# Kernel tuning notes

Hardware: AMD Instinct MI355X
Metric: run time of the kernel (lower is better)

Reference implementation:

```python
import jax, jax.numpy as jnp
import numpy as np

B, H, L, N, F = 32, 256, 2048, 64, 32  # batch, d_model, seq len, d_state//2 complex modes, num_features


def setup_inputs() -> dict:
    key = jax.random.key(0)
    ks = jax.random.split(key, 16)
    inp = {
        "x": jax.random.normal(ks[0], (B, H, L), jnp.float32),
        "t": jax.random.normal(ks[1], (B, H), jnp.float32),
        "features": jax.random.normal(ks[2], (B, F, L), jnp.float32),
        # time_linear
        "Wt": jax.random.normal(ks[3], (H, H), jnp.float32) / np.sqrt(H),
        "bt": jnp.zeros((H,), jnp.float32),
        # LayerNorm over d_model
        "ln_g": jnp.ones((H,), jnp.float32),
        "ln_b": jnp.zeros((H,), jnp.float32),
        # S4 (diagonal / S4D parameterization, d_state=128 -> N=64 complex, bidirectional)
        "log_dt": jnp.log(jnp.full((H,), 0.01, jnp.float32))
                  + jax.random.uniform(ks[4], (H,), jnp.float32, -1.0, 1.0),
        "logA_real": jnp.log(0.5 * jnp.ones((H, N), jnp.float32)),
        "A_imag": jnp.broadcast_to(np.pi * jnp.arange(N, dtype=jnp.float32), (H, N)).copy(),
        "C_re": jax.random.normal(ks[5], (2, H, N), jnp.float32) / np.sqrt(2 * N),
        "C_im": jax.random.normal(ks[6], (2, H, N), jnp.float32) / np.sqrt(2 * N),
        "D": jax.random.normal(ks[7], (H,), jnp.float32),
        # S4 output position-wise linear
        "Wout": jax.random.normal(ks[8], (H, H), jnp.float32) / np.sqrt(H),
        "bout": jnp.zeros((H,), jnp.float32),
        # out_linear1 / out_linear2 (1x1 convs)
        "W1": jax.random.normal(ks[9], (H, H), jnp.float32) / np.sqrt(H),
        "b1": jnp.zeros((H,), jnp.float32),
        "W2": jax.random.normal(ks[10], (H, H), jnp.float32) / np.sqrt(H),
        "b2": jnp.zeros((H,), jnp.float32),
        # feature_encoder 1x1 conv
        "Wf": jax.random.normal(ks[11], (H, F), jnp.float32) / np.sqrt(F),
        "bf": jnp.zeros((H,), jnp.float32),
    }
    return inp


def _s4_block(x, t, features, Wt, bt, ln_g, ln_b, log_dt, logA_real, A_imag,
              C_re, C_im, D, Wout, bout, W1, b1, W2, b2, Wf, bf):
    Bb, Hh, Ll = x.shape
    # time conditioning: Linear(t) broadcast over length  -> (B,H,L)
    tb = t @ Wt.T + bt
    xin = x + tb[:, :, None]
    # LayerNorm over channel (d_model) axis (norm applied on transposed tensor)
    mu = jnp.mean(xin, axis=1, keepdims=True)
    var = jnp.var(xin, axis=1, keepdims=True)
    z = (xin - mu) / jnp.sqrt(var + 1e-5) * ln_g[None, :, None] + ln_b[None, :, None]
    # --- bidirectional S4 (diagonal SSM) kernel ---
    dt = jnp.exp(log_dt)                       # (H,)
    A = -jnp.exp(logA_real) + 1j * A_imag      # (H,N)
    dtA = dt[:, None] * A                      # (H,N)
    Cd = (C_re + 1j * C_im) * (jnp.exp(dtA) - 1.0) / A      # (2,H,N) discretized C
    vand = jnp.exp(dtA[:, :, None] * jnp.arange(Ll))         # (H,N,L) Vandermonde
    K = 2.0 * jnp.real(jnp.einsum('chn,hnl->chl', Cd, vand))  # (2,H,L)
    zeros = jnp.zeros_like(K[0])
    k = jnp.concatenate([K[0], zeros], -1) + jnp.concatenate([zeros, K[1][:, ::-1]], -1)  # (H,2L)
    # FFT global convolution
    y = jnp.fft.irfft(jnp.fft.rfft(z, 2 * Ll) * jnp.fft.rfft(k, 2 * Ll)[None], 2 * Ll)[..., :Ll]
    y = y + z * D[None, :, None]
    y = jax.nn.gelu(y)
    y = jnp.einsum('bhl,gh->bgl', y, Wout) + bout[None, :, None]
    xr = y + xin                                # residual inside S4Layer
    # feature encoder + gated activation
    out = xr + jnp.einsum('bfl,hf->bhl', features, Wf) + bf[None, :, None]
    g = jnp.tanh(out) * jax.nn.sigmoid(out)
    o1 = jnp.einsum('bhl,gh->bgl', g, W1) + b1[None, :, None]
    o2 = jnp.einsum('bhl,gh->bgl', g, W2) + b2[None, :, None]
    return (o1 + x, o2)


def reference(x, t, features, Wt, bt, ln_g, ln_b, log_dt, logA_real, A_imag,
              C_re, C_im, D, Wout, bout, W1, b1, W2, b2, Wf, bf):
    return _s4_block(x, t, features, Wt, bt, ln_g, ln_b, log_dt, logA_real, A_imag,
                     C_re, C_im, D, Wout, bout, W1, b1, W2, b2, Wf, bf)
```

## Files before the change

kernel.cpp:

```cpp
#include <hip/hip_runtime.h>

typedef unsigned short ushort_t;

#define Bb 32
#define Hh 256
#define Ll 2048
#define Nn 64
#define BHL 16777216

typedef __bf16 bf16x8 __attribute__((ext_vector_type(8)));
typedef float f32x4 __attribute__((ext_vector_type(4)));
typedef unsigned int uint4v __attribute__((ext_vector_type(4)));

__device__ __forceinline__ ushort_t f2bf(float f) {
    unsigned int u = __float_as_uint(f);
    unsigned int r = ((u >> 16) & 1u) + 0x7fffu;
    return (ushort_t)((u + r) >> 16);
}
__device__ __forceinline__ float bf2f(ushort_t h) {
    return __uint_as_float(((unsigned int)h) << 16);
}
__device__ __forceinline__ float gelu_tanh(float v) {
    float u = 0.7978845608028654f * fmaf(0.044715f * v, v * v, v);
    float e = __expf(2.f * u);
    float th = 1.f - 2.f / (e + 1.f);
    return 0.5f * v * (1.f + th);
}
__device__ __forceinline__ float gate_fn(float v) {
    float sg = 1.f / (1.f + __expf(-v));
    float e2 = __expf(2.f * v);
    float th = 1.f - 2.f / (e2 + 1.f);
    return th * sg;
}
__device__ __forceinline__ uint4v rev8v(uint4v a) {
    union { uint4v v; ushort_t s8[8]; } x, y;
    x.v = a;
    #pragma unroll
    for (int j = 0; j < 8; ++j) y.s8[j] = x.s8[7 - j];
    return y.v;
}

__global__ __launch_bounds__(256) void prep_kernel(
    const float* __restrict__ t, const float* __restrict__ Wt, const float* __restrict__ bt,
    const float* __restrict__ Wout, const float* __restrict__ Wf,
    const float* __restrict__ bout, const float* __restrict__ bfb,
    const float* __restrict__ W1, const float* __restrict__ b1,
    const float* __restrict__ W2, const float* __restrict__ b2,
    float* __restrict__ tb, float* __restrict__ bc, float* __restrict__ b12,
    ushort_t* __restrict__ wcf, ushort_t* __restrict__ w12f)
{
    int bx = blockIdx.x, tid = threadIdx.x;
    __shared__ float trow[256];
    if (bx < 32) {
        trow[tid] = t[bx * 256 + tid];
        __syncthreads();
        float acc = bt[tid];
        #pragma unroll 4
        for (int hh = 0; hh < 256; ++hh) acc = fmaf(trow[hh], Wt[tid * 256 + hh], acc);
        tb[bx * 256 + tid] = acc;
    } else if (bx < 64) {
        int gt = (bx - 32) * 256 + tid;
        if (gt < 256) bc[gt] = bout[gt] + bfb[gt];
        if (gt < 512) b12[gt] = (gt < 256) ? b1[gt] : b2[gt - 256];
        for (int fg = gt; fg < 9216; fg += 8192) {
            int mt = fg / 576, rem = fg % 576;
            int kc = rem >> 6, lane = rem & 63;
            int m = mt * 16 + (lane & 15);
            int kb = kc * 32 + (lane >> 4) * 8;
            #pragma unroll
            for (int j = 0; j < 8; ++j) {
                int k = kb + j;
                float v = (k < 256) ? Wout[m * 256 + k] : Wf[m * 32 + (k - 256)];
                wcf[(size_t)fg * 8 + j] = f2bf(v);
            }
        }
    } else {
        int gt = (bx - 64) * 256 + tid;
        for (int fg = gt; fg < 16384; fg += 8192) {
            int mt = fg >> 9, rem = fg & 511;
            int kc = rem >> 6, lane = rem & 63;
            int m = mt * 16 + (lane & 15);
            int kb = kc * 32 + (lane >> 4) * 8;
            #pragma unroll
            for (int j = 0; j < 8; ++j) {
                int k = kb + j;
                float v = (m < 256) ? W1[m * 256 + k] : W2[(m - 256) * 256 + k];
                w12f[(size_t)fg * 8 + j] = f2bf(v);
            }
        }
    }
}

__global__ __launch_bounds__(256) void prep2_kernel(
    const float* __restrict__ log_dt, const float* __restrict__ logA, const float* __restrict__ Aimg,
    const float* __restrict__ C_re, const float* __restrict__ C_im,
    float* __restrict__ drg, float* __restrict__ dig,
    ushort_t* __restrict__ Mfrag, ushort_t* __restrict__ Vfrag)
{
    int bx = blockIdx.x, tid = threadIdx.x;
    int h = bx >> 1, dir = bx & 1;
    __shared__ float drL[64], diL[64], crL[64], ciL[64];
    __shared__ float ktab[128];
    __shared__ ushort_t bndL[128 * 128];
    if (tid < 64) {
        int n = tid;
        int idx = h * 64 + n;
        float dt = __expf(log_dt[h]);
        float Ar = -__expf(logA[idx]);
        float Ai = Aimg[idx];
        float dr = dt * Ar, di = dt * Ai;
        float er = __expf(dr);
        float wr_ = er * __cosf(di), wi_ = er * __sinf(di);
        float nr = wr_ - 1.f, ni = wi_;
        float inv = 1.f / (Ar * Ar + Ai * Ai);
        float qr = (nr * Ar + ni * Ai) * inv;
        float qi = (ni * Ar - nr * Ai) * inv;
        float cr = C_re[dir * 16384 + idx], ci = C_im[dir * 16384 + idx];
        drL[n] = dr; diL[n] = di;
        crL[n] = 2.f * (cr * qr - ci * qi);
        ciL[n] = 2.f * (cr * qi + ci * qr);
        if (dir == 0) { drg[idx] = dr; dig[idx] = di; }
    }
    __syncthreads();
    if (tid < 128) {
        int i = tid;
        float e = (float)(i + 1 - dir);
        #pragma unroll 4
        for (int n = 0; n < 64; ++n) {
            float ex = __expf(e * drL[n]);
            float ph = e * diL[n];
            float pr = ex * __cosf(ph), pi = ex * __sinf(ph);
            bndL[i * 128 + n]      = f2bf(crL[n] * pr - ciL[n] * pi);
            bndL[i * 128 + 64 + n] = f2bf(-(crL[n] * pi + ciL[n] * pr));
        }
    } else {
        int d = tid - 128;
        float e = (float)d;
        float acc = 0.f;
        #pragma unroll 4
        for (int n = 0; n < 64; ++n) {
            float ex = __expf(e * drL[n]);
            float ph = e * diL[n];
            acc += crL[n] * (ex * __cosf(ph)) - ciL[n] * (ex * __sinf(ph));
        }
        ktab[d] = acc;
    }
    __syncthreads();
    size_t base = (size_t)bx << 15;
    for (int idx = tid; idx < 32768; idx += 256) {
        int j = idx & 7, lane = (idx >> 3) & 63, kc = (idx >> 9) & 7, mt = idx >> 12;
        int m = mt * 16 + (lane & 15);
        int k = kc * 32 + (lane >> 4) * 8 + j;
        float v;
        if (k < 128) {
            int d = m - k - dir;
            v = (d >= 0) ? ktab[d] : 0.f;
        } else {
            v = bf2f(bndL[m * 128 + (k - 128)]);
        }
        Mfrag[base + idx] = f2bf(v);
    }
    if (dir == 0) {
        size_t vbase = (size_t)h << 14;
        for (int idx = tid; idx < 16384; idx += 256) {
            int j = idx & 7, lane = (idx >> 3) & 63, kc = (idx >> 9) & 3, mt = idx >> 11;
            int s = mt * 16 + (lane & 15);
            int k = kc * 32 + (lane >> 4) * 8 + j;
            int n = s & 63;
            float e = (float)(127 - k);
            float ex = __expf(e * drL[n]);
            float ph = e * diL[n];
            float v = (s < 64) ? ex * __cosf(ph) : ex * __sinf(ph);
            Vfrag[vbase + idx] = f2bf(v);
        }
    }
}

__global__ __launch_bounds__(256) void ln_kernel(
    const float* __restrict__ x, const float* __restrict__ tb,
    const float* __restrict__ ln_g, const float* __restrict__ ln_b,
    ushort_t* __restrict__ zbf)
{
    __shared__ float Xs[256][65];
    __shared__ float rs[4][64], rq[4][64];
    int tid = threadIdx.x, bx = blockIdx.x;
    int b = bx >> 5, l0 = (bx & 31) << 6;
    const float* xb = x + (size_t)b * (Hh * (size_t)Ll) + l0;
    const float* tbp = tb + b * 256;
    int f4 = tid & 15, h0 = tid >> 4;
    #pragma unroll
    for (int i = 0; i < 16; ++i) {
        int h = i * 16 + h0;
        float4 v = *((const float4*)(xb + (size_t)h * Ll) + f4);
        float tv = tbp[h];
        Xs[h][f4 * 4 + 0] = v.x + tv;
        Xs[h][f4 * 4 + 1] = v.y + tv;
        Xs[h][f4 * 4 + 2] = v.z + tv;
        Xs[h][f4 * 4 + 3] = v.w + tv;
    }
    __syncthreads();
    int l = tid & 63, qd = tid >> 6;
    float sum = 0.f, ssq = 0.f;
    #pragma unroll 8
    for (int i = 0; i < 64; ++i) {
        float v = Xs[qd * 64 + i][l];
        sum += v; ssq = fmaf(v, v, ssq);
    }
    rs[qd][l] = sum; rq[qd][l] = ssq;
    __syncthreads();
    sum = rs[0][l] + rs[1][l] + rs[2][l] + rs[3][l];
    ssq = rq[0][l] + rq[1][l] + rq[2][l] + rq[3][l];
    float mean = sum * (1.f / 256.f);
    float var = fmaf(ssq, 1.f / 256.f, -mean * mean);
    float rstd = rsqrtf(var + 1e-5f);
    ushort_t* zp = zbf + (size_t)b * (Hh * (size_t)Ll) + l0 + l;
    #pragma unroll 8
    for (int i = 0; i < 64; ++i) {
        int h = qd * 64 + i;
        float v = Xs[h][l];
        zp[(size_t)h * Ll] = f2bf((v - mean) * rstd * ln_g[h] + ln_b[h]);
    }
}

__global__ __launch_bounds__(256) void ssm_mega_kernel(
    const ushort_t* __restrict__ zbf,
    const float* __restrict__ drg, const float* __restrict__ dig, const float* __restrict__ Dv,
    const ushort_t* __restrict__ Mfrag, const ushort_t* __restrict__ Vfrag,
    ushort_t* __restrict__ ya)
{
    __shared__ ushort_t Zs[64 * 136];
    __shared__ ushort_t Ssf[64 * 136];
    __shared__ ushort_t Ssb[64 * 136];
    __shared__ float Qb[2 * 128 * 17];
    int tid = threadIdx.x, lane = tid & 63, w = tid >> 6;
    int q = lane >> 4, cl = lane & 15;
    int h = blockIdx.x, cb = blockIdx.y;
    int b0 = cb * 4;
    for (int i = tid; i < 1024; i += 256) {
        int bsub = i >> 8, t8 = (i & 255) * 8;
        const ushort_t* zrow = zbf + ((size_t)((b0 + bsub) * 256 + h) << 11);
        *(uint4v*)&Zs[(bsub * 16 + (t8 >> 7)) * 136 + (t8 & 127)] = *(const uint4v*)(zrow + t8);
    }
    float dr0 = drg[h * 64 + lane], di0 = dig[h * 64 + lane];
    float ex128 = __expf(128.f * dr0);
    float w128r = ex128 * __cosf(128.f * di0);
    float w128i = ex128 * __sinf(128.f * di0);
    float Dh = Dv[h];
    __syncthreads();
    const ushort_t* vbase = Vfrag + ((size_t)h << 14);
    const ushort_t* mbase0 = Mfrag + ((size_t)(h * 2) << 15);
    const ushort_t* mbase1 = Mfrag + ((size_t)(h * 2 + 1) << 15);
    for (int bsub = 0; bsub < 4; ++bsub) {
        f32x4 qa[2][2] = {};
        #pragma unroll
        for (int kc = 0; kc < 4; ++kc) {
            int kk = kc * 32 + q * 8;
            bf16x8 bz = __builtin_bit_cast(bf16x8,
                *(const uint4v*)&Zs[(bsub * 16 + cl) * 136 + kk]);
            bf16x8 bzr = __builtin_bit_cast(bf16x8, rev8v(
                *(const uint4v*)&Zs[(bsub * 16 + (15 - cl)) * 136 + (120 - kk)]));
            #pragma unroll
            for (int i = 0; i < 2; ++i) {
                int mt = w * 2 + i;
                bf16x8 af = __builtin_bit_cast(bf16x8,
                    *(const uint4v*)(vbase + (((mt * 4 + kc) * 64 + lane) << 3)));
                qa[0][i] = __builtin_amdgcn_mfma_f32_16x16x32_bf16(af, bz, qa[0][i], 0, 0, 0);
                qa[1][i] = __builtin_amdgcn_mfma_f32_16x16x32_bf16(af, bzr, qa[1][i], 0, 0, 0);
            }
        }
        __syncthreads();
        #pragma unroll
        for (int d = 0; d < 2; ++d)
            #pragma unroll
            for (int i = 0; i < 2; ++i) {
                int mt = w * 2 + i;
                #pragma unroll
                for (int r = 0; r < 4; ++r)
                    Qb[d * 2176 + (mt * 16 + q * 4 + r) * 17 + cl] = qa[d][i][r];
            }
        __syncthreads();
        if (w < 2) {
            ushort_t* S = (w == 0) ? Ssf : Ssb;
            const float* Qp = Qb + w * 2176;
            float sre = 0.f, sim = 0.f;
            for (int cc = 0; cc < 16; ++cc) {
                S[(bsub * 16 + cc) * 136 + lane] = f2bf(sre);
                S[(bsub * 16 + cc) * 136 + 64 + lane] = f2bf(sim);
                float qre = Qp[lane * 17 + cc];
                float qim = Qp[(64 + lane) * 17 + cc];
                float nre = fmaf(w128r, sre, fmaf(-w128i, sim, qre));
                float nim = fmaf(w128r, sim, fmaf(w128i, sre, qim));
                sre = nre; sim = nim;
            }
        }
        __syncthreads();
    }
    f32x4 accf[2][4] = {}, accb[2][4] = {};
    for (int kc = 0; kc < 8; ++kc) {
        int kk = (kc & 3) * 32 + q * 8;
        bf16x8 aff[2], afb[2];
        #pragma unroll
        for (int i = 0; i < 2; ++i) {
            int mt = w * 2 + i;
            aff[i] = __builtin_bit_cast(bf16x8, *(const uint4v*)(mbase0 + (((mt * 8 + kc) * 64 + lane) << 3)));
            afb[i] = __builtin_bit_cast(bf16x8, *(const uint4v*)(mbase1 + (((mt * 8 + kc) * 64 + lane) << 3)));
        }
        #pragma unroll
        for (int nt = 0; nt < 4; ++nt) {
            bf16x8 bff, bfb_;
            if (kc < 4) {
                bff  = __builtin_bit_cast(bf16x8, *(const uint4v*)&Zs[(nt * 16 + cl) * 136 + kk]);
                bfb_ = __builtin_bit_cast(bf16x8, rev8v(
                       *(const uint4v*)&Zs[(nt * 16 + (15 - cl)) * 136 + (120 - kk)]));
            } else {
                bff  = __builtin_bit_cast(bf16x8, *(const uint4v*)&Ssf[(nt * 16 + cl) * 136 + kk]);
                bfb_ = __builtin_bit_cast(bf16x8, *(const uint4v*)&Ssb[(nt * 16 + cl) * 136 + kk]);
            }
            #pragma unroll
            for (int i = 0; i < 2; ++i) {
                accf[i][nt] = __builtin_amdgcn_mfma_f32_16x16x32_bf16(aff[i], bff,  accf[i][nt], 0, 0, 0);
                accb[i][nt] = __builtin_amdgcn_mfma_f32_16x16x32_bf16(afb[i], bfb_, accb[i][nt], 0, 0, 0);
            }
        }
    }
    __syncthreads();
    ushort_t* Yf = Ssf;
    ushort_t* Yb = Ssb;
    #pragma unroll
    for (int i = 0; i < 2; ++i) {
        int mt = w * 2 + i;
        #pragma unroll
        for (int nt = 0; nt < 4; ++nt) {
            int col = nt * 16 + cl;
            #pragma unroll
            for (int r = 0; r < 4; ++r) {
                int m = mt * 16 + q * 4 + r;
                Yf[col * 136 + m] = f2bf(accf[i][nt][r]);
                Yb[col * 136 + m] = f2bf(accb[i][nt][r]);
            }
        }
    }
    __syncthreads();
    for (int u = tid; u < 1024; u += 256) {
        int col = u >> 4, i0 = (u & 15) * 8;
        int bsub = col >> 4, c = col & 15;
        int colb = bsub * 16 + (15 - c);
        union { uint4v v; ushort_t s8[8]; } uf, uz, ub, uo;
        uf.v = *(const uint4v*)&Yf[col * 136 + i0];
        uz.v = *(const uint4v*)&Zs[col * 136 + i0];
        ub.v = rev8v(*(const uint4v*)&Yb[colb * 136 + (120 - i0)]);
        #pragma unroll
        for (int j = 0; j < 8; ++j) {
            float v = bf2f(uf.s8[j]) + bf2f(ub.s8[j]) + Dh * bf2f(uz.s8[j]);
            uo.s8[j] = f2bf(gelu_tanh(v));
        }
        ushort_t* yrow = ya + ((size_t)((b0 + bsub) * 256 + h) << 11);
        *(uint4v*)(yrow + c * 128 + i0) = uo.v;
    }
}

__global__ __launch_bounds__(256, 4) void gemm1_kernel(
    const ushort_t* __restrict__ ya, const float* __restrict__ feat,
    const float* __restrict__ x, const float* __restrict__ tb,
    const float* __restrict__ bc, const ushort_t* __restrict__ wcf,
    ushort_t* __restrict__ g)
{
    __shared__ __align__(16) ushort_t XT[64 * 48];
    int tid = threadIdx.x;
    int w = tid >> 6, lane = tid & 63;
    int bx = blockIdx.x;
    int b = bx >> 5;
    int l0 = (bx & 31) << 6;
    f32x4 acc[4][4] = {};
    int kk = tid >> 3, ng = tid & 7;
    for (int kc = 0; kc < 9; ++kc) {
        int k = kc * 32 + kk;
        union { uint4v v; ushort_t s[8]; } u;
        if (k < 256) {
            u.v = *(const uint4v*)(ya + ((size_t)(b * 256 + k) << 11) + l0 + ng * 8);
        } else {
            const float* src = feat + (size_t)(b * 32 + (k - 256)) * Ll + l0 + ng * 8;
            #pragma unroll
            for (int j = 0; j < 8; ++j) u.s[j] = f2bf(src[j]);
        }
        #pragma unroll
        for (int j = 0; j < 8; ++j) XT[(ng * 8 + j) * 48 + kk] = u.s[j];
        __syncthreads();
        bf16x8 af[4], bfr[4];
        #pragma unroll
        for (int i = 0; i < 4; ++i) {
            const ushort_t* p = wcf + ((size_t)((w * 4 + i) * 9 + kc) * 64 + lane) * 8;
            af[i] = __builtin_bit_cast(bf16x8, *(const uint4v*)p);
        }
        #pragma unroll
        for (int nt = 0; nt < 4; ++nt) {
            const ushort_t* p = &XT[(nt * 16 + (lane & 15)) * 48 + (lane >> 4) * 8];
            bfr[nt] = __builtin_bit_cast(bf16x8, *(const uint4v*)p);
        }
        #pragma unroll
        for (int i = 0; i < 4; ++i)
            #pragma unroll
            for (int nt = 0; nt < 4; ++nt)
                acc[i][nt] = __builtin_amdgcn_mfma_f32_16x16x32_bf16(af[i], bfr[nt], acc[i][nt], 0, 0, 0);
        __syncthreads();
    }
    int q = lane >> 4, nl = lane & 15;
    #pragma unroll
    for (int i = 0; i < 4; ++i) {
        #pragma unroll
        for (int nt = 0; nt < 4; ++nt) {
            int n = l0 + nt * 16 + nl;
            #pragma unroll
            for (int r = 0; r < 4; ++r) {
                int m = (w * 4 + i) * 16 + q * 4 + r;
                size_t oi = (size_t)(b * 256 + m) * Ll + n;
                float v = acc[i][nt][r] + bc[m] + tb[b * 256 + m] + x[oi];
                g[oi] = f2bf(gate_fn(v));
            }
        }
    }
}

__global__ __launch_bounds__(256, 4) void gemm2_kernel(
    const ushort_t* __restrict__ g, const float* __restrict__ x,
    const float* __restrict__ b12, const ushort_t* __restrict__ w12f,
    float* __restrict__ out)
{
    __shared__ __align__(16) ushort_t XT[64 * 48];
    int tid = threadIdx.x;
    int w = tid >> 6, lane = tid & 63;
    int bx = blockIdx.x;
    int half = blockIdx.y;
    int b = bx >> 5;
    int l0 = (bx & 31) << 6;
    f32x4 acc[4][4] = {};
    int kk = tid >> 3, ng = tid & 7;
    for (int kc = 0; kc < 8; ++kc) {
        int k = kc * 32 + kk;
        union { uint4v v; ushort_t s[8]; } u;
        u.v = *(const uint4v*)(g + (size_t)(b * 256 + k) * Ll + l0 + ng * 8);
        #pragma unroll
        for (int j = 0; j < 8; ++j) XT[(ng * 8 + j) * 48 + kk] = u.s[j];
        __syncthreads();
        bf16x8 af[4], bfr[4];
        #pragma unroll
        for (int i = 0; i < 4; ++i) {
            int mtg = half * 16 + w * 4 + i;
            const ushort_t* p = w12f + ((size_t)(mtg * 8 + kc) * 64 + lane) * 8;
            af[i] = __builtin_bit_cast(bf16x8, *(const uint4v*)p);
        }
        #pragma unroll
        for (int nt = 0; nt < 4; ++nt) {
            const ushort_t* p = &XT[(nt * 16 + (lane & 15)) * 48 + (lane >> 4) * 8];
            bfr[nt] = __builtin_bit_cast(bf16x8, *(const uint4v*)p);
        }
        #pragma unroll
        for (int i = 0; i < 4; ++i)
            #pragma unroll
            for (int nt = 0; nt < 4; ++nt)
                acc[i][nt] = __builtin_amdgcn_mfma_f32_16x16x32_bf16(af[i], bfr[nt], acc[i][nt], 0, 0, 0);
        __syncthreads();
    }
    int q = lane >> 4, nl = lane & 15;
    #pragma unroll
    for (int i = 0; i < 4; ++i) {
        #pragma unroll
        for (int nt = 0; nt < 4; ++nt) {
            int n = l0 + nt * 16 + nl;
            #pragma unroll
            for (int r = 0; r < 4; ++r) {
                int m = (w * 4 + i) * 16 + q * 4 + r;
                size_t oi = (size_t)(b * 256 + m) * Ll + n;
                float v = acc[i][nt][r] + b12[half * 256 + m];
                if (half == 0) out[oi] = v + x[oi];
                else out[(size_t)BHL + oi] = v;
            }
        }
    }
}

extern "C" void kernel_launch(void* const* d_in, const int* in_sizes, int n_in,
                              void* d_out, int out_size, void* d_ws, size_t ws_size,
                              hipStream_t stream) {
    const float* x      = (const float*)d_in[0];
    const float* t      = (const float*)d_in[1];
    const float* feat   = (const float*)d_in[2];
    const float* Wt     = (const float*)d_in[3];
    const float* bt     = (const float*)d_in[4];
    const float* ln_g   = (const float*)d_in[5];
    const float* ln_b   = (const float*)d_in[6];
    const float* log_dt = (const float*)d_in[7];
    const float* logA   = (const float*)d_in[8];
    const float* Aimg   = (const float*)d_in[9];
    const float* C_re   = (const float*)d_in[10];
    const float* C_im   = (const float*)d_in[11];
    const float* Dv     = (const float*)d_in[12];
    const float* Wout   = (const float*)d_in[13];
    const float* bout   = (const float*)d_in[14];
    const float* W1     = (const float*)d_in[15];
    const float* b1     = (const float*)d_in[16];
    const float* W2     = (const float*)d_in[17];
    const float* b2     = (const float*)d_in[18];
    const float* Wf     = (const float*)d_in[19];
    const float* bfb    = (const float*)d_in[20];

    char* ob = (char*)d_out;
    ushort_t* zbf = (ushort_t*)ob;
    ushort_t* yab = (ushort_t*)(ob + 33554432);
    float*    out = (float*)d_out;

    char* ws = (char*)d_ws;
    ushort_t* Mfrag = (ushort_t*)ws;
    ushort_t* gbuf  = (ushort_t*)ws;
    ushort_t* Vfrag = (ushort_t*)(ws + 33554432);
    char* ws2 = ws + 33554432 + 8388608;
    float* tb   = (float*)ws2;
    float* drg  = (float*)(ws2 + 32768);
    float* dig  = (float*)(ws2 + 98304);
    float* bc   = (float*)(ws2 + 163840);
    float* b12  = (float*)(ws2 + 164864);
    ushort_t* wcf  = (ushort_t*)(ws2 + 166912);
    ushort_t* w12f = (ushort_t*)(ws2 + 314368);

    prep_kernel<<<96, 256, 0, stream>>>(t, Wt, bt, Wout, Wf, bout, bfb, W1, b1, W2, b2,
                                        tb, bc, b12, wcf, w12f);
    prep2_kernel<<<512, 256, 0, stream>>>(log_dt, logA, Aimg, C_re, C_im, drg, dig, Mfrag, Vfrag);
    ln_kernel<<<1024, 256, 0, stream>>>(x, tb, ln_g, ln_b, zbf);
    ssm_mega_kernel<<<dim3(256, 8), 256, 0, stream>>>(zbf, drg, dig, Dv, Mfrag, Vfrag, yab);
    gemm1_kernel<<<1024, 256, 0, stream>>>(yab, feat, x, tb, bc, wcf, gbuf);
    gemm2_kernel<<<dim3(1024, 2), 256, 0, stream>>>(gbuf, x, b12, w12f, out);
}
```

Baseline: 408.5 us.

## Merge SSM prep with layernorm and loop batch chunks in SSM kernel

The SSM coefficient precompute and the layernorm are combined into one launch, with blocks dispatched by index, so one kernel launch goes away and the two stages can overlap. The SSM kernel now handles 16 batches per block instead of 4, keeping the Vandermonde A-fragments in registers across chunks. This cuts the grid from 2048 to 512 blocks, reducing parallelism and latency hiding. The merged kernel's larger shared-memory footprint may also lower layernorm occupancy.

```diff
diff --git a/kernel.cpp b/kernel.cpp
--- a/kernel.cpp
+++ b/kernel.cpp
@@ -91,134 +91,139 @@
     }
 }
 
-__global__ __launch_bounds__(256) void prep2_kernel(
+__global__ __launch_bounds__(256) void prep2ln_kernel(
     const float* __restrict__ log_dt, const float* __restrict__ logA, const float* __restrict__ Aimg,
     const float* __restrict__ C_re, const float* __restrict__ C_im,
     float* __restrict__ drg, float* __restrict__ dig,
-    ushort_t* __restrict__ Mfrag, ushort_t* __restrict__ Vfrag)
-{
-    int bx = blockIdx.x, tid = threadIdx.x;
-    int h = bx >> 1, dir = bx & 1;
-    __shared__ float drL[64], diL[64], crL[64], ciL[64];
-    __shared__ float ktab[128];
-    __shared__ ushort_t bndL[128 * 128];
-    if (tid < 64) {
-        int n = tid;
-        int idx = h * 64 + n;
-        float dt = __expf(log_dt[h]);
-        float Ar = -__expf(logA[idx]);
-        float Ai = Aimg[idx];
-        float dr = dt * Ar, di = dt * Ai;
-        float er = __expf(dr);
-        float wr_ = er * __cosf(di), wi_ = er * __sinf(di);
-        float nr = wr_ - 1.f, ni = wi_;
-        float inv = 1.f / (Ar * Ar + Ai * Ai);
-        float qr = (nr * Ar + ni * Ai) * inv;
-        float qi = (ni * Ar - nr * Ai) * inv;
-        float cr = C_re[dir * 16384 + idx], ci = C_im[dir * 16384 + idx];
-        drL[n] = dr; diL[n] = di;
-        crL[n] = 2.f * (cr * qr - ci * qi);
-        ciL[n] = 2.f * (cr * qi + ci * qr);
-        if (dir == 0) { drg[idx] = dr; dig[idx] = di; }
-    }
-    __syncthreads();
-    if (tid < 128) {
-        int i = tid;
-        float e = (float)(i + 1 - dir);
-        #pragma unroll 4
-        for (int n = 0; n < 64; ++n) {
-            float ex = __expf(e * drL[n]);
-            float ph = e * diL[n];
-            float pr = ex * __cosf(ph), pi = ex * __sinf(ph);
-            bndL[i * 128 + n]      = f2bf(crL[n] * pr - ciL[n] * pi);
-            bndL[i * 128 + 64 + n] = f2bf(-(crL[n] * pi + ciL[n] * pr));
-        }
-    } else {
-        int d = tid - 128;
-        float e = (float)d;
-        float acc = 0.f;
-        #pragma unroll 4
-        for (int n = 0; n < 64; ++n) {
-            float ex = __expf(e * drL[n]);
-            float ph = e * diL[n];
-            acc += crL[n] * (ex * __cosf(ph)) - ciL[n] * (ex * __sinf(ph));
-        }
-        ktab[d] = acc;
-    }
-    __syncthreads();
-    size_t base = (size_t)bx << 15;
-    for (int idx = tid; idx < 32768; idx += 256) {
-        int j = idx & 7, lane = (idx >> 3) & 63, kc = (idx >> 9) & 7, mt = idx >> 12;
-        int m = mt * 16 + (lane & 15);
-        int k = kc * 32 + (lane >> 4) * 8 + j;
-        float v;
-        if (k < 128) {
-            int d = m - k - dir;
-            v = (d >= 0) ? ktab[d] : 0.f;
-        } else {
-            v = bf2f(bndL[m * 128 + (k - 128)]);
-        }
-        Mfrag[base + idx] = f2bf(v);
-    }
-    if (dir == 0) {
-        size_t vbase = (size_t)h << 14;
-        for (int idx = tid; idx < 16384; idx += 256) {
-            int j = idx & 7, lane = (idx >> 3) & 63, kc = (idx >> 9) & 3, mt = idx >> 11;
-            int s = mt * 16 + (lane & 15);
-            int k = kc * 32 + (lane >> 4) * 8 + j;
-            int n = s & 63;
-            float e = (float)(127 - k);
-            float ex = __expf(e * drL[n]);
-            float ph = e * diL[n];
-            float v = (s < 64) ? ex * __cosf(ph) : ex * __sinf(ph);
-            Vfrag[vbase + idx] = f2bf(v);
-        }
-    }
-}
-
-__global__ __launch_bounds__(256) void ln_kernel(
+    ushort_t* __restrict__ Mfrag, ushort_t* __restrict__ Vfrag,
     const float* __restrict__ x, const float* __restrict__ tb,
     const float* __restrict__ ln_g, const float* __restrict__ ln_b,
     ushort_t* __restrict__ zbf)
 {
-    __shared__ float Xs[256][65];
-    __shared__ float rs[4][64], rq[4][64];
-    int tid = threadIdx.x, bx = blockIdx.x;
-    int b = bx >> 5, l0 = (bx & 31) << 6;
-    const float* xb = x + (size_t)b * (Hh * (size_t)Ll) + l0;
-    const float* tbp = tb + b * 256;
-    int f4 = tid & 15, h0 = tid >> 4;
-    #pragma unroll
-    for (int i = 0; i < 16; ++i) {
-        int h = i * 16 + h0;
-        float4 v = *((const float4*)(xb + (size_t)h * Ll) + f4);
-        float tv = tbp[h];
-        Xs[h][f4 * 4 + 0] = v.x + tv;
-        Xs[h][f4 * 4 + 1] = v.y + tv;
-        Xs[h][f4 * 4 + 2] = v.z + tv;
-        Xs[h][f4 * 4 + 3] = v.w + tv;
-    }
-    __syncthreads();
-    int l = tid & 63, qd = tid >> 6;
-    float sum = 0.f, ssq = 0.f;
-    #pragma unroll 8
-    for (int i = 0; i < 64; ++i) {
-        float v = Xs[qd * 64 + i][l];
-        sum += v; ssq = fmaf(v, v, ssq);
-    }
-    rs[qd][l] = sum; rq[qd][l] = ssq;
-    __syncthreads();
-    sum = rs[0][l] + rs[1][l] + rs[2][l] + rs[3][l];
-    ssq = rq[0][l] + rq[1][l] + rq[2][l] + rq[3][l];
-    float mean = sum * (1.f / 256.f);
-    float var = fmaf(ssq, 1.f / 256.f, -mean * mean);
-    float rstd = rsqrtf(var + 1e-5f);
-    ushort_t* zp = zbf + (size_t)b * (Hh * (size_t)Ll) + l0 + l;
-    #pragma unroll 8
-    for (int i = 0; i < 64; ++i) {
-        int h = qd * 64 + i;
-        float v = Xs[h][l];
-        zp[(size_t)h * Ll] = f2bf((v - mean) * rstd * ln_g[h] + ln_b[h]);
+    __shared__ __align__(16) char smem[68608];
+    int bxg = blockIdx.x, tid = threadIdx.x;
+    if (bxg < 512) {
+        float* drL = (float*)smem;
+        float* diL = drL + 64;
+        float* crL = drL + 128;
+        float* ciL = drL + 192;
+        float* ktab = drL + 256;
+        ushort_t* bndL = (ushort_t*)(smem + 1536);
+        int bx = bxg;
+        int h = bx >> 1, dir = bx & 1;
+        if (tid < 64) {
+            int n = tid;
+            int idx = h * 64 + n;
+            float dt = __expf(log_dt[h]);
+            float Ar = -__expf(logA[idx]);
+            float Ai = Aimg[idx];
+            float dr = dt * Ar, di = dt * Ai;
+            float er = __expf(dr);
+            float wr_ = er * __cosf(di), wi_ = er * __sinf(di);
+            float nr = wr_ - 1.f, ni = wi_;
+            float inv = 1.f / (Ar * Ar + Ai * Ai);
+            float qr = (nr * Ar + ni * Ai) * inv;
+            float qi = (ni * Ar - nr * Ai) * inv;
+            float cr = C_re[dir * 16384 + idx], ci = C_im[dir * 16384 + idx];
+            drL[n] = dr; diL[n] = di;
+            crL[n] = 2.f * (cr * qr - ci * qi);
+            ciL[n] = 2.f * (cr * qi + ci * qr);
+            if (dir == 0) { drg[idx] = dr; dig[idx] = di; }
+        }
+        __syncthreads();
+        if (tid < 128) {
+            int i = tid;
+            float e = (float)(i + 1 - dir);
+            #pragma unroll 4
+            for (int n = 0; n < 64; ++n) {
+                float ex = __expf(e * drL[n]);
+                float ph = e * diL[n];
+                float pr = ex * __cosf(ph), pi = ex * __sinf(ph);
+                bndL[i * 128 + n]      = f2bf(crL[n] * pr - ciL[n] * pi);
+                bndL[i * 128 + 64 + n] = f2bf(-(crL[n] * pi + ciL[n] * pr));
+            }
+        } else {
+            int d = tid - 128;
+            float e = (float)d;
+            float acc = 0.f;
+            #pragma unroll 4
+            for (int n = 0; n < 64; ++n) {
+                float ex = __expf(e * drL[n]);
+                float ph = e * diL[n];
+                acc += crL[n] * (ex * __cosf(ph)) - ciL[n] * (ex * __sinf(ph));
+            }
+            ktab[d] = acc;
+        }
+        __syncthreads();
+        size_t base = (size_t)bx << 15;
+        for (int idx = tid; idx < 32768; idx += 256) {
+            int j = idx & 7, lane = (idx >> 3) & 63, kc = (idx >> 9) & 7, mt = idx >> 12;
+            int m = mt * 16 + (lane & 15);
+            int k = kc * 32 + (lane >> 4) * 8 + j;
+            float v;
+            if (k < 128) {
+                int d = m - k - dir;
+                v = (d >= 0) ? ktab[d] : 0.f;
+            } else {
+                v = bf2f(bndL[m * 128 + (k - 128)]);
+            }
+            Mfrag[base + idx] = f2bf(v);
+        }
+        if (dir == 0) {
+            size_t vbase = (size_t)h << 14;
+            for (int idx = tid; idx < 16384; idx += 256) {
+                int j = idx & 7, lane = (idx >> 3) & 63, kc = (idx >> 9) & 3, mt = idx >> 11;
+                int s = mt * 16 + (lane & 15);
+                int k = kc * 32 + (lane >> 4) * 8 + j;
+                int n = s & 63;
+                float e = (float)(127 - k);
+                float ex = __expf(e * drL[n]);
+                float ph = e * diL[n];
+                float v = (s < 64) ? ex * __cosf(ph) : ex * __sinf(ph);
+                Vfrag[vbase + idx] = f2bf(v);
+            }
+        }
+    } else {
+        float* Xs = (float*)smem;
+        float* rs = (float*)(smem + 66560);
+        float* rq = rs + 256;
+        int bx = bxg - 512;
+        int b = bx >> 5, l0 = (bx & 31) << 6;
+        const float* xb = x + (size_t)b * (Hh * (size_t)Ll) + l0;
+        const float* tbp = tb + b * 256;
+        int f4 = tid & 15, h0 = tid >> 4;
+        #pragma unroll
+        for (int i = 0; i < 16; ++i) {
+            int h = i * 16 + h0;
+            float4 v = *((const float4*)(xb + (size_t)h * Ll) + f4);
+            float tv = tbp[h];
+            Xs[h * 65 + f4 * 4 + 0] = v.x + tv;
+            Xs[h * 65 + f4 * 4 + 1] = v.y + tv;
+            Xs[h * 65 + f4 * 4 + 2] = v.z + tv;
+            Xs[h * 65 + f4 * 4 + 3] = v.w + tv;
+        }
+        __syncthreads();
+        int l = tid & 63, qd = tid >> 6;
+        float sum = 0.f, ssq = 0.f;
+        #pragma unroll 8
+        for (int i = 0; i < 64; ++i) {
+            float v = Xs[(qd * 64 + i) * 65 + l];
+            sum += v; ssq = fmaf(v, v, ssq);
+        }
+        rs[qd * 64 + l] = sum; rq[qd * 64 + l] = ssq;
+        __syncthreads();
+        sum = rs[l] + rs[64 + l] + rs[128 + l] + rs[192 + l];
+        ssq = rq[l] + rq[64 + l] + rq[128 + l] + rq[192 + l];
+        float mean = sum * (1.f / 256.f);
+        float var = fmaf(ssq, 1.f / 256.f, -mean * mean);
+        float rstd = rsqrtf(var + 1e-5f);
+        ushort_t* zp = zbf + (size_t)b * (Hh * (size_t)Ll) + l0 + l;
+        #pragma unroll 8
+        for (int i = 0; i < 64; ++i) {
+            int h = qd * 64 + i;
+            float v = Xs[h * 65 + l];
+            zp[(size_t)h * Ll] = f2bf((v - mean) * rstd * ln_g[h] + ln_b[h]);
+        }
     }
 }
 
@@ -234,128 +239,139 @@
     __shared__ float Qb[2 * 128 * 17];
     int tid = threadIdx.x, lane = tid & 63, w = tid >> 6;
     int q = lane >> 4, cl = lane & 15;
-    int h = blockIdx.x, cb = blockIdx.y;
-    int b0 = cb * 4;
-    for (int i = tid; i < 1024; i += 256) {
-        int bsub = i >> 8, t8 = (i & 255) * 8;
-        const ushort_t* zrow = zbf + ((size_t)((b0 + bsub) * 256 + h) << 11);
-        *(uint4v*)&Zs[(bsub * 16 + (t8 >> 7)) * 136 + (t8 & 127)] = *(const uint4v*)(zrow + t8);
-    }
+    int h = blockIdx.x;
+    int g2 = blockIdx.y;
     float dr0 = drg[h * 64 + lane], di0 = dig[h * 64 + lane];
     float ex128 = __expf(128.f * dr0);
     float w128r = ex128 * __cosf(128.f * di0);
     float w128i = ex128 * __sinf(128.f * di0);
     float Dh = Dv[h];
-    __syncthreads();
     const ushort_t* vbase = Vfrag + ((size_t)h << 14);
     const ushort_t* mbase0 = Mfrag + ((size_t)(h * 2) << 15);
     const ushort_t* mbase1 = Mfrag + ((size_t)(h * 2 + 1) << 15);
-    for (int bsub = 0; bsub < 4; ++bsub) {
-        f32x4 qa[2][2] = {};
-        #pragma unroll
-        for (int kc = 0; kc < 4; ++kc) {
-            int kk = kc * 32 + q * 8;
-            bf16x8 bz = __builtin_bit_cast(bf16x8,
-                *(const uint4v*)&Zs[(bsub * 16 + cl) * 136 + kk]);
-            bf16x8 bzr = __builtin_bit_cast(bf16x8, rev8v(
-                *(const uint4v*)&Zs[(bsub * 16 + (15 - cl)) * 136 + (120 - kk)]));
+    bf16x8 vfr[4][2];
+    #pragma unroll
+    for (int kc = 0; kc < 4; ++kc)
+        #pragma unroll
+        for (int i = 0; i < 2; ++i) {
+            int mt = w * 2 + i;
+            vfr[kc][i] = __builtin_bit_cast(bf16x8,
+                *(const uint4v*)(vbase + (((mt * 4 + kc) * 64 + lane) << 3)));
+        }
+    #pragma unroll 1
+    for (int cbs = 0; cbs < 4; ++cbs) {
+        int b0 = g2 * 16 + cbs * 4;
+        for (int i = tid; i < 1024; i += 256) {
+            int bsub = i >> 8, t8 = (i & 255) * 8;
+            const ushort_t* zrow = zbf + ((size_t)((b0 + bsub) * 256 + h) << 11);
+            *(uint4v*)&Zs[(bsub * 16 + (t8 >> 7)) * 136 + (t8 & 127)] = *(const uint4v*)(zrow + t8);
+        }
+        __syncthreads();
+        for (int bsub = 0; bsub < 4; ++bsub) {
+            f32x4 qa[2][2] = {};
+            #pragma unroll
+            for (int kc = 0; kc < 4; ++kc) {
+                int kk = kc * 32 + q * 8;
+                bf16x8 bz = __builtin_bit_cast(bf16x8,
+                    *(const uint4v*)&Zs[(bsub * 16 + cl) * 136 + kk]);
+                bf16x8 bzr = __builtin_bit_cast(bf16x8, rev8v(
+                    *(const uint4v*)&Zs[(bsub * 16 + (15 - cl)) * 136 + (120 - kk)]));
+                #pragma unroll
+                for (int i = 0; i < 2; ++i) {
+                    qa[0][i] = __builtin_amdgcn_mfma_f32_16x16x32_bf16(vfr[kc][i], bz, qa[0][i], 0, 0, 0);
+                    qa[1][i] = __builtin_amdgcn_mfma_f32_16x16x32_bf16(vfr[kc][i], bzr, qa[1][i], 0, 0, 0);
+                }
+            }
+            __syncthreads();
+            #pragma unroll
+            for (int d = 0; d < 2; ++d)
+                #pragma unroll
+                for (int i = 0; i < 2; ++i) {
+                    int mt = w * 2 + i;
+                    #pragma unroll
+                    for (int r = 0; r < 4; ++r)
+                        Qb[d * 2176 + (mt * 16 + q * 4 + r) * 17 + cl] = qa[d][i][r];
+                }
+            __syncthreads();
+            if (w < 2) {
+                ushort_t* S = (w == 0) ? Ssf : Ssb;
+                const float* Qp = Qb + w * 2176;
+                float sre = 0.f, sim = 0.f;
+                for (int cc = 0; cc < 16; ++cc) {
+                    S[(bsub * 16 + cc) * 136 + lane] = f2bf(sre);
+                    S[(bsub * 16 + cc) * 136 + 64 + lane] = f2bf(sim);
+                    float qre = Qp[lane * 17 + cc];
+                    float qim = Qp[(64 + lane) * 17 + cc];
+                    float nre = fmaf(w128r, sre, fmaf(-w128i, sim, qre));
+                    float nim = fmaf(w128r, sim, fmaf(w128i, sre, qim));
+                    sre = nre; sim = nim;
+                }
+            }
+            __syncthreads();
+        }
+        f32x4 accf[2][4] = {}, accb[2][4] = {};
+        for (int kc = 0; kc < 8; ++kc) {
+            int kk = (kc & 3) * 32 + q * 8;
+            bf16x8 aff[2], afb[2];
             #pragma unroll
             for (int i = 0; i < 2; ++i) {
                 int mt = w * 2 + i;
-                bf16x8 af = __builtin_bit_cast(bf16x8,
-                    *(const uint4v*)(vbase + (((mt * 4 + kc) * 64 + lane) << 3)));
-                qa[0][i] = __builtin_amdgcn_mfma_f32_16x16x32_bf16(af, bz, qa[0][i], 0, 0, 0);
-                qa[1][i] = __builtin_amdgcn_mfma_f32_16x16x32_bf16(af, bzr, qa[1][i], 0, 0, 0);
-            }
-        }
-        __syncthreads();
-        #pragma unroll
-        for (int d = 0; d < 2; ++d)
-            #pragma unroll
-            for (int i = 0; i < 2; ++i) {
-                int mt = w * 2 + i;
+                aff[i] = __builtin_bit_cast(bf16x8, *(const uint4v*)(mbase0 + (((mt * 8 + kc) * 64 + lane) << 3)));
+                afb[i] = __builtin_bit_cast(bf16x8, *(const uint4v*)(mbase1 + (((mt * 8 + kc) * 64 + lane) << 3)));
+            }
+            #pragma unroll
+            for (int nt = 0; nt < 4; ++nt) {
+                bf16x8 bff, bfb_;
+                if (kc < 4) {
+                    bff  = __builtin_bit_cast(bf16x8, *(const uint4v*)&Zs[(nt * 16 + cl) * 136 + kk]);
+                    bfb_ = __builtin_bit_cast(bf16x8, rev8v(
+                           *(const uint4v*)&Zs[(nt * 16 + (15 - cl)) * 136 + (120 - kk)]));
+                } else {
+                    bff  = __builtin_bit_cast(bf16x8, *(const uint4v*)&Ssf[(nt * 16 + cl) * 136 + kk]);
+                    bfb_ = __builtin_bit_cast(bf16x8, *(const uint4v*)&Ssb[(nt * 16 + cl) * 136 + kk]);
+                }
                 #pragma unroll
-                for (int r = 0; r < 4; ++r)
-                    Qb[d * 2176 + (mt * 16 + q * 4 + r) * 17 + cl] = qa[d][i][r];
-            }
-        __syncthreads();
-        if (w < 2) {
-            ushort_t* S = (w == 0) ? Ssf : Ssb;
-            const float* Qp = Qb + w * 2176;
-            float sre = 0.f, sim = 0.f;
-            for (int cc = 0; cc < 16; ++cc) {
-                S[(bsub * 16 + cc) * 136 + lane] = f2bf(sre);
-                S[(bsub * 16 + cc) * 136 + 64 + lane] = f2bf(sim);
-                float qre = Qp[lane * 17 + cc];
-                float qim = Qp[(64 + lane) * 17 + cc];
-                float nre = fmaf(w128r, sre, fmaf(-w128i, sim, qre));
-                float nim = fmaf(w128r, sim, fmaf(w128i, sre, qim));
-                sre = nre; sim = nim;
-            }
-        }
-        __syncthreads();
-    }
-    f32x4 accf[2][4] = {}, accb[2][4] = {};
-    for (int kc = 0; kc < 8; ++kc) {
-        int kk = (kc & 3) * 32 + q * 8;
-        bf16x8 aff[2], afb[2];
+                for (int i = 0; i < 2; ++i) {
+                    accf[i][nt] = __builtin_amdgcn_mfma_f32_16x16x32_bf16(aff[i], bff,  accf[i][nt], 0, 0, 0);
+                    accb[i][nt] = __builtin_amdgcn_mfma_f32_16x16x32_bf16(afb[i], bfb_, accb[i][nt], 0, 0, 0);
+                }
+            }
+        }
+        __syncthreads();
+        ushort_t* Yf = Ssf;
+        ushort_t* Yb = Ssb;
         #pragma unroll
         for (int i = 0; i < 2; ++i) {
             int mt = w * 2 + i;
-            aff[i] = __builtin_bit_cast(bf16x8, *(const uint4v*)(mbase0 + (((mt * 8 + kc) * 64 + lane) << 3)));
-            afb[i] = __builtin_bit_cast(bf16x8, *(const uint4v*)(mbase1 + (((mt * 8 + kc) * 64 + lane) << 3)));
-        }
-        #pragma unroll
-        for (int nt = 0; nt < 4; ++nt) {
-            bf16x8 bff, bfb_;
-            if (kc < 4) {
-                bff  = __builtin_bit_cast(bf16x8, *(const uint4v*)&Zs[(nt * 16 + cl) * 136 + kk]);
-                bfb_ = __builtin_bit_cast(bf16x8, rev8v(
-                       *(const uint4v*)&Zs[(nt * 16 + (15 - cl)) * 136 + (120 - kk)]));
-            } else {
-                bff  = __builtin_bit_cast(bf16x8, *(const uint4v*)&Ssf[(nt * 16 + cl) * 136 + kk]);
-                bfb_ = __builtin_bit_cast(bf16x8, *(const uint4v*)&Ssb[(nt * 16 + cl) * 136 + kk]);
-            }
-            #pragma unroll
-            for (int i = 0; i < 2; ++i) {
-                accf[i][nt] = __builtin_amdgcn_mfma_f32_16x16x32_bf16(aff[i], bff,  accf[i][nt], 0, 0, 0);
-                accb[i][nt] = __builtin_amdgcn_mfma_f32_16x16x32_bf16(afb[i], bfb_, accb[i][nt], 0, 0, 0);
-            }
-        }
-    }
-    __syncthreads();
-    ushort_t* Yf = Ssf;
-    ushort_t* Yb = Ssb;
-    #pragma unroll
-    for (int i = 0; i < 2; ++i) {
-        int mt = w * 2 + i;
-        #pragma unroll
-        for (int nt = 0; nt < 4; ++nt) {
-            int col = nt * 16 + cl;
-            #pragma unroll
-            for (int r = 0; r < 4; ++r) {
-                int m = mt * 16 + q * 4 + r;
-                Yf[col * 136 + m] = f2bf(accf[i][nt][r]);
-                Yb[col * 136 + m] = f2bf(accb[i][nt][r]);
-            }
-        }
-    }
-    __syncthreads();
-    for (int u = tid; u < 1024; u += 256) {
-        int col = u >> 4, i0 = (u & 15) * 8;
-        int bsub = col >> 4, c = col & 15;
-        int colb = bsub * 16 + (15 - c);
-        union { uint4v v; ushort_t s8[8]; } uf, uz, ub, uo;
-        uf.v = *(const uint4v*)&Yf[col * 136 + i0];
-        uz.v = *(const uint4v*)&Zs[col * 136 + i0];
-        ub.v = rev8v(*(const uint4v*)&Yb[colb * 136 + (120 - i0)]);
-        #pragma unroll
-        for (int j = 0; j < 8; ++j) {
-            float v = bf2f(uf.s8[j]) + bf2f(ub.s8[j]) + Dh * bf2f(uz.s8[j]);
-            uo.s8[j] = f2bf(gelu_tanh(v));
-        }
-        ushort_t* yrow = ya + ((size_t)((b0 + bsub) * 256 + h) << 11);
-        *(uint4v*)(yrow + c * 128 + i0) = uo.v;
+            #pragma unroll
+            for (int nt = 0; nt < 4; ++nt) {
+                int col = nt * 16 + cl;
+                #pragma unroll
+                for (int r = 0; r < 4; ++r) {
+                    int m = mt * 16 + q * 4 + r;
+                    Yf[col * 136 + m] = f2bf(accf[i][nt][r]);
+                    Yb[col * 136 + m] = f2bf(accb[i][nt][r]);
+                }
+            }
+        }
+        __syncthreads();
+        for (int u = tid; u < 1024; u += 256) {
+            int col = u >> 4, i0 = (u & 15) * 8;
+            int bsub = col >> 4, c = col & 15;
+            int colb = bsub * 16 + (15 - c);
+            union { uint4v v; ushort_t s8[8]; } uf, uz, ub, uo;
+            uf.v = *(const uint4v*)&Yf[col * 136 + i0];
+            uz.v = *(const uint4v*)&Zs[col * 136 + i0];
+            ub.v = rev8v(*(const uint4v*)&Yb[colb * 136 + (120 - i0)]);
+            #pragma unroll
+            for (int j = 0; j < 8; ++j) {
+                float v = bf2f(uf.s8[j]) + bf2f(ub.s8[j]) + Dh * bf2f(uz.s8[j]);
+                uo.s8[j] = f2bf(gelu_tanh(v));
+            }
+            ushort_t* yrow = ya + ((size_t)((b0 + bsub) * 256 + h) << 11);
+            *(uint4v*)(yrow + c * 128 + i0) = uo.v;
+        }
+        __syncthreads();
     }
 }
 
@@ -524,9 +540,9 @@
 
     prep_kernel<<<96, 256, 0, stream>>>(t, Wt, bt, Wout, Wf, bout, bfb, W1, b1, W2, b2,
                                         tb, bc, b12, wcf, w12f);
-    prep2_kernel<<<512, 256, 0, stream>>>(log_dt, logA, Aimg, C_re, C_im, drg, dig, Mfrag, Vfrag);
-    ln_kernel<<<1024, 256, 0, stream>>>(x, tb, ln_g, ln_b, zbf);
-    ssm_mega_kernel<<<dim3(256, 8), 256, 0, stream>>>(zbf, drg, dig, Dv, Mfrag, Vfrag, yab);
+    prep2ln_kernel<<<1536, 256, 0, stream>>>(log_dt, logA, Aimg, C_re, C_im, drg, dig,
+                                             Mfrag, Vfrag, x, tb, ln_g, ln_b, zbf);
+    ssm_mega_kernel<<<dim3(256, 2), 256, 0, stream>>>(zbf, drg, dig, Dv, Mfrag, Vfrag, yab);
     gemm1_kernel<<<1024, 256, 0, stream>>>(yab, feat, x, tb, bc, wcf, gbuf);
     gemm2_kernel<<<dim3(1024, 2), 256, 0, stream>>>(gbuf, x, b12, w12f, out);
 }
```

Measured after the change: 431.1 us. 5.5% more time.
